# Optimization experiments

Measured on AMD Instinct MI355X. Metric: run time of the kernel, lower is better.

## Reference

```python
import jax, jax.numpy as jnp
import numpy as np

N, D, R, E = 50000, 256, 4, 800000
LN_EPS = 1e-5
NEG_INF = -1e30  # finite stand-in for -inf so softmax stays grad-safe


def _layernorm(x, g, b):
    m = x.mean(axis=-1, keepdims=True)
    v = x.var(axis=-1, keepdims=True)
    return (x - m) / jnp.sqrt(v + LN_EPS) * g + b


def setup_inputs() -> dict:
    key = jax.random.key(0)
    ks = jax.random.split(key, 8)
    s = 1.0 / np.sqrt(D).astype(np.float32)
    return {
        'rows': jax.random.randint(ks[0], (R, E), 0, N),
        'cols': jax.random.randint(ks[1], (R, E), 0, N),
        'vals': jax.random.uniform(ks[2], (R, E), jnp.float32),
        'node_emb': jax.random.normal(ks[3], (N, D), jnp.float32) * s,
        'pre_W': jax.random.normal(ks[4], (D, D), jnp.float32) * s,
        'pre_b': jnp.zeros((D,), jnp.float32),
        'ln1_g': jnp.ones((D,), jnp.float32),
        'ln1_b': jnp.zeros((D,), jnp.float32),
        'rel_W': jax.random.normal(ks[5], (R, D, D), jnp.float32) * s,
        'attn_vec': jax.random.normal(ks[6], (D,), jnp.float32) * s,
        'self_W': jax.random.normal(ks[7], (D, D), jnp.float32) * s,
        'self_b': jnp.zeros((D,), jnp.float32),
        'bias': jnp.zeros((D,), jnp.float32),
        'ln2_g': jnp.ones((D,), jnp.float32),
        'ln2_b': jnp.zeros((D,), jnp.float32),
    }


def reference(rows, cols, vals, node_emb, pre_W, pre_b, ln1_g, ln1_b, rel_W,
              attn_vec, self_W, self_b, bias, ln2_g, ln2_b):
    # active_indices = arange(N), so x_all is the full embedding table
    x_all = node_emb
    # pre_encoder: Linear -> LayerNorm -> GELU (exact erf, torch default)
    x = jax.nn.gelu(_layernorm(x_all @ pre_W + pre_b, ln1_g, ln1_b), approximate=False)
    # per-relation: relation linear then SpMM (adj_t @ x_rel) via gather + segment_sum
    msgs = []
    for i in range(R):
        x_rel = x @ rel_W[i]                              # [N, D]
        contrib = vals[i][:, None] * x_rel[cols[i]]       # [E, D]
        msgs.append(jax.ops.segment_sum(contrib, rows[i], num_segments=N))
    stacked = jnp.stack(msgs, axis=1)                     # [N, R, D]
    # semantic attention over relations
    scores = jnp.einsum('nrd,d->nr', stacked, attn_vec)   # [N, R]
    mask = jnp.any(stacked != 0, axis=2)                  # [N, R]
    attn = jax.nn.softmax(jnp.where(mask, scores, NEG_INF), axis=1)
    attn = attn * mask                                    # == nan_to_num(softmax(-inf rows))
    out = jnp.einsum('nrd,nr->nd', stacked, attn) + bias + (x @ self_W + self_b)
    out = jax.nn.gelu(out, approximate=False)
    # active_indices = arange(N): scatter into global index space is identity
    final = _layernorm(out, ln2_g, ln2_b)
    return final, attn, x_all
```

## Files before the change

kernel.cpp:

```cpp
#include <hip/hip_runtime.h>
#include <math.h>


typedef __attribute__((ext_vector_type(8))) short bf16x8;
typedef __attribute__((ext_vector_type(4))) float f32x4;
typedef unsigned long long u64;

__device__ __forceinline__ float gelu_exact(float v) {
    return 0.5f * v * (1.0f + erff(v * 0.70710678118654752f));
}
__device__ __forceinline__ unsigned short f2bf(float f) {
    unsigned u = __float_as_uint(f);
    return (unsigned short)((u + 0x7fffu + ((u >> 16) & 1u)) >> 16);
}
__device__ __forceinline__ unsigned pack2(float a, float b) {
    return (unsigned)f2bf(a) | ((unsigned)f2bf(b) << 16);
}
__device__ __forceinline__ void gload16(const void* g, void* l) {
    __builtin_amdgcn_global_load_lds(
        (const __attribute__((address_space(1))) void*)g,
        (__attribute__((address_space(3))) void*)l, 16, 0, 0);
}

__global__ __launch_bounds__(256)
void conv_emb(const float* __restrict__ ne, unsigned short* __restrict__ emb,
              float* __restrict__ outX, int total4)
{
    const int stride = gridDim.x * blockDim.x;
    for (int i = blockIdx.x * blockDim.x + threadIdx.x; i < total4; i += stride) {
        const float4 v = reinterpret_cast<const float4*>(ne)[i];
        reinterpret_cast<float4*>(outX)[i] = v;
        ushort4 h;
        h.x = f2bf(v.x); h.y = f2bf(v.y); h.z = f2bf(v.z); h.w = f2bf(v.w);
        reinterpret_cast<ushort4*>(emb)[i] = h;
    }
}

__global__ __launch_bounds__(256)
void build_bt(const float* __restrict__ relW, const float* __restrict__ selfW,
              const float* __restrict__ preW, unsigned short* __restrict__ BTm,
              unsigned short* __restrict__ BTp)
{
    const int idx = blockIdx.x * 256 + threadIdx.x;
    if (idx < 1280 * 256) {
        const int k = idx >> 8, n = idx & 255;
        const float v = (k < 1024)
            ? relW[(size_t)(k >> 8) * 65536 + (size_t)(k & 255) * 256 + n]
            : selfW[(size_t)(k - 1024) * 256 + n];
        BTm[(size_t)n * 1280 + k] = f2bf(v);
    } else {
        const int i2 = idx - 1280 * 256;
        if (i2 < 256 * 256) {
            const int k = i2 >> 8, n = i2 & 255;
            BTp[(size_t)n * 256 + k] = f2bf(preW[(size_t)k * 256 + n]);
        }
    }
}

template<int MODE>
__global__ __launch_bounds__(512)
void gemm_mfma(const unsigned short* __restrict__ a0,
               const unsigned short* __restrict__ a1,
               const unsigned short* __restrict__ a2,
               const unsigned short* __restrict__ a3,
               const unsigned short* __restrict__ a4,
               const unsigned short* __restrict__ BT,
               const float* __restrict__ bias0, const float* __restrict__ bias1,
               const float* __restrict__ lng, const float* __restrict__ lnb,
               float* __restrict__ Cout, unsigned short* __restrict__ XOut,
               int M)
{
    constexpr int K    = MODE ? 1280 : 256;
    constexpr int NSEG = MODE ? 5 : 1;

    __shared__ __align__(16) unsigned char smA[128 * 128];
    __shared__ __align__(16) unsigned char smB[256 * 128];
    __shared__ float redS[4][128];
    __shared__ float redQ[4][128];

    const int tid = threadIdx.x;
    const int w   = tid >> 6;
    const int l   = tid & 63;
    const int wm  = w >> 2, wn = w & 3;
    const int brow = blockIdx.x * 128;

    const int srow = l >> 3;
    const int sgA  = (l & 7) ^ srow;

    f32x4 acc[4][4];
#pragma unroll
    for (int mb = 0; mb < 4; ++mb)
#pragma unroll
        for (int nb = 0; nb < 4; ++nb)
            acc[mb][nb] = f32x4{0.f, 0.f, 0.f, 0.f};

    for (int seg = 0; seg < NSEG; ++seg) {
        const unsigned short* Abase =
            (MODE == 0) ? a0
                        : (seg == 0 ? a0 : seg == 1 ? a1 : seg == 2 ? a2
                                         : seg == 3 ? a3 : a4);
#pragma unroll
        for (int kk = 0; kk < 4; ++kk) {
            __syncthreads();
#pragma unroll
            for (int c = 0; c < 2; ++c) {
                const int r0 = (w * 2 + c) * 8;
                int gm = brow + r0 + srow;
                gm = min(gm, M - 1);
                gload16(Abase + ((size_t)gm << 8) + kk * 64 + sgA * 8,
                        smA + (w * 2 + c) * 1024);
            }
#pragma unroll
            for (int c = 0; c < 4; ++c) {
                const int bn = (w * 4 + c) * 8 + srow;
                gload16(BT + (size_t)bn * K + (seg * 4 + kk) * 64 + sgA * 8,
                        smB + (w * 4 + c) * 1024);
            }
            __syncthreads();

#pragma unroll
            for (int ks = 0; ks < 2; ++ks) {
                bf16x8 af[4], bf[4];
#pragma unroll
                for (int mb = 0; mb < 4; ++mb) {
                    const int row = wm * 64 + mb * 16 + (l & 15);
                    const int g   = (ks * 4 + (l >> 4)) ^ (row & 7);
                    af[mb] = *reinterpret_cast<const bf16x8*>(smA + row * 128 + g * 16);
                }
#pragma unroll
                for (int nb = 0; nb < 4; ++nb) {
                    const int row = wn * 64 + nb * 16 + (l & 15);
                    const int g   = (ks * 4 + (l >> 4)) ^ (row & 7);
                    bf[nb] = *reinterpret_cast<const bf16x8*>(smB + row * 128 + g * 16);
                }
#pragma unroll
                for (int mb = 0; mb < 4; ++mb)
#pragma unroll
                    for (int nb = 0; nb < 4; ++nb)
                        acc[mb][nb] = __builtin_amdgcn_mfma_f32_16x16x32_bf16(
                            af[mb], bf[nb], acc[mb][nb], 0, 0, 0);
            }
        }
    }

    float bb[4], gw[4], bw[4];
#pragma unroll
    for (int nb = 0; nb < 4; ++nb) {
        const int n = wn * 64 + nb * 16 + (l & 15);
        bb[nb] = bias0[n] + (MODE == 1 ? bias1[n] : 0.0f);
        gw[nb] = lng[n];
        bw[nb] = lnb[n];
    }
#pragma unroll
    for (int mb = 0; mb < 4; ++mb)
#pragma unroll
        for (int nb = 0; nb < 4; ++nb)
#pragma unroll
            for (int rg = 0; rg < 4; ++rg) {
                float v = acc[mb][nb][rg] + bb[nb];
                if (MODE == 1) v = gelu_exact(v);
                acc[mb][nb][rg] = v;
            }
#pragma unroll
    for (int mb = 0; mb < 4; ++mb)
#pragma unroll
        for (int rg = 0; rg < 4; ++rg) {
            float s = 0.f, q = 0.f;
#pragma unroll
            for (int nb = 0; nb < 4; ++nb) {
                const float v = acc[mb][nb][rg];
                s += v; q += v * v;
            }
#pragma unroll
            for (int off = 1; off < 16; off <<= 1) {
                s += __shfl_xor(s, off, 64);
                q += __shfl_xor(q, off, 64);
            }
            if ((l & 15) == 0) {
                const int row = wm * 64 + mb * 16 + (l >> 4) * 4 + rg;
                redS[wn][row] = s;
                redQ[wn][row] = q;
            }
        }
    __syncthreads();
    if (tid < 128) {
        const float s = redS[0][tid] + redS[1][tid] + redS[2][tid] + redS[3][tid];
        const float q = redQ[0][tid] + redQ[1][tid] + redQ[2][tid] + redQ[3][tid];
        const float mean = s * (1.0f / 256.0f);
        const float var  = q * (1.0f / 256.0f) - mean * mean;
        redS[0][tid] = mean;
        redQ[0][tid] = rsqrtf(var + 1e-5f);
    }
    __syncthreads();
#pragma unroll
    for (int mb = 0; mb < 4; ++mb)
#pragma unroll
        for (int rg = 0; rg < 4; ++rg) {
            const int row = wm * 64 + mb * 16 + (l >> 4) * 4 + rg;
            if (brow + row >= M) continue;
            const float mu = redS[0][row];
            const float rs = redQ[0][row];
#pragma unroll
            for (int nb = 0; nb < 4; ++nb) {
                const int n = wn * 64 + nb * 16 + (l & 15);
                const float v = (acc[mb][nb][rg] - mu) * rs * gw[nb] + bw[nb];
                if (MODE == 0)
                    XOut[((size_t)(brow + row) << 8) + n] = f2bf(gelu_exact(v));
                else
                    Cout[((size_t)(brow + row) << 8) + n] = v;
            }
        }
}

__global__ __launch_bounds__(256)
void wtilde_kernel(const float* __restrict__ relW, const float* __restrict__ av,
                   float* __restrict__ wt)
{
    __shared__ float avs[256];
    const int r = blockIdx.x, tid = threadIdx.x;
    avs[tid] = av[tid];
    __syncthreads();
    const float* W = relW + (size_t)r * 65536 + (size_t)tid * 256;
    float s = 0.f;
    for (int j = 0; j < 256; j += 4) {
        const float4 w4 = *reinterpret_cast<const float4*>(W + j);
        s += w4.x * avs[j] + w4.y * avs[j + 1] + w4.z * avs[j + 2] + w4.w * avs[j + 3];
    }
    wt[r * 256 + tid] = s;
}

__global__ __launch_bounds__(256)
void y_kernel(const unsigned short* __restrict__ XB, const float* __restrict__ wt,
              float* __restrict__ y, int Nn)
{
    const int n = blockIdx.x * 4 + (threadIdx.x >> 6);
    if (n >= Nn) return;
    const int l = threadIdx.x & 63;
    const uint2 d = *reinterpret_cast<const uint2*>(XB + ((size_t)n << 8) + l * 4);
    float xv[4];
    xv[0] = __uint_as_float(d.x << 16);
    xv[1] = __uint_as_float(d.x & 0xffff0000u);
    xv[2] = __uint_as_float(d.y << 16);
    xv[3] = __uint_as_float(d.y & 0xffff0000u);
    float s[4];
#pragma unroll
    for (int r = 0; r < 4; ++r) {
        const float4 w4 = *reinterpret_cast<const float4*>(wt + r * 256 + l * 4);
        s[r] = xv[0] * w4.x + xv[1] * w4.y + xv[2] * w4.z + xv[3] * w4.w;
#pragma unroll
        for (int off = 32; off; off >>= 1) s[r] += __shfl_xor(s[r], off, 64);
    }
    if (l == 0)
        *reinterpret_cast<float4*>(y + (size_t)n * 4) = make_float4(s[0], s[1], s[2], s[3]);
}

__global__ __launch_bounds__(256)
void hist_widbin(const int* __restrict__ rows, int* __restrict__ counts,
                 int* __restrict__ cnt_t, int RE, int E, int Nn,
                 int chunk, int NBIN)
{
    __shared__ int lh[800];
    const int blk = blockIdx.x;
    for (int i = threadIdx.x; i < NBIN; i += 256) lh[i] = 0;
    __syncthreads();
    const int e0 = blk * chunk;
    const int e1 = min(e0 + chunk, RE);
    for (int e = e0 + threadIdx.x; e < e1; e += 256) {
        const int r   = e / E;
        const int wid = r * Nn + rows[e];
        atomicAdd(&counts[wid], 1);
        atomicAdd(&lh[wid >> 8], 1);
    }
    __syncthreads();
    for (int i = threadIdx.x; i < NBIN; i += 256)
        cnt_t[i * gridDim.x + blk] = lh[i];
}

__global__ __launch_bounds__(256)
void scan_blocks(const int* __restrict__ counts, int* __restrict__ offs,
                 int* __restrict__ bsums, int n)
{
    __shared__ int sh[256];
    const int t = threadIdx.x;
    const int base = blockIdx.x * 1024 + t * 4;
    int v[4], s = 0;
#pragma unroll
    for (int j = 0; j < 4; ++j) {
        v[j] = (base + j < n) ? counts[base + j] : 0;
        s += v[j];
    }
    sh[t] = s;
    __syncthreads();
    for (int off = 1; off < 256; off <<= 1) {
        const int x = (t >= off) ? sh[t - off] : 0;
        __syncthreads();
        sh[t] += x;
        __syncthreads();
    }
    int run = sh[t] - s;
    if (t == 255) bsums[blockIdx.x] = sh[255];
#pragma unroll
    for (int j = 0; j < 4; ++j) {
        if (base + j < n) offs[base + j] = run;
        run += v[j];
    }
}

__global__ __launch_bounds__(256)
void scan_bsums(int* __restrict__ bsums, int nblk)
{
    __shared__ int sh[256];
    const int t = threadIdx.x;
    const int v = (t < nblk) ? bsums[t] : 0;
    sh[t] = v;
    __syncthreads();
    for (int off = 1; off < 256; off <<= 1) {
        const int x = (t >= off) ? sh[t - off] : 0;
        __syncthreads();
        sh[t] += x;
        __syncthreads();
    }
    if (t < nblk) bsums[t] = sh[t] - v;
}

__global__ __launch_bounds__(256)
void scan_add(int* __restrict__ offs, const int* __restrict__ bsums, int n)
{
    const int i = blockIdx.x * 256 + threadIdx.x;
    if (i >= n) return;
    offs[i] += bsums[i >> 10];
}

__global__ __launch_bounds__(256)
void scatter_coarse(const int* __restrict__ rows, const int* __restrict__ cols,
                    const float* __restrict__ vals, const int* __restrict__ ctoffs,
                    u64* __restrict__ edc, int RE, int E, int Nn,
                    int chunk, int NBIN)
{
    __shared__ int lcur[800];
    const int blk = blockIdx.x;
    for (int i = threadIdx.x; i < NBIN; i += 256)
        lcur[i] = ctoffs[i * gridDim.x + blk];
    __syncthreads();
    const int e0 = blk * chunk;
    const int e1 = min(e0 + chunk, RE);
    for (int e = e0 + threadIdx.x; e < e1; e += 256) {
        const int r   = e / E;
        const int row = rows[e];
        const int wid = r * Nn + row;
        const int pos = atomicAdd(&lcur[wid >> 8], 1);
        const unsigned vb = __float_as_uint(vals[e]);
        edc[pos] = ((u64)((vb & 0xFFFFFFFCu) | (unsigned)r) << 32)
                 | ((unsigned)row << 16) | (unsigned)cols[e];
    }
}

__global__ __launch_bounds__(256)
void scatter_fine(const u64* __restrict__ edc, const int* __restrict__ ctoffs,
                  const int* __restrict__ offs, u64* __restrict__ edata,
                  int RE, int Nn, int NB1, int NBIN)
{
    __shared__ int cur[256];
    const int bin     = blockIdx.x;
    const int widbase = bin << 8;
    const int RN      = Nn << 2;
    const int wid     = widbase + threadIdx.x;
    cur[threadIdx.x] = (wid < RN) ? offs[wid] : 0;
    __syncthreads();
    const int cs = ctoffs[bin * NB1];
    const int ce = (bin + 1 < NBIN) ? ctoffs[(bin + 1) * NB1] : RE;
    for (int j = cs + threadIdx.x; j < ce; j += 256) {
        const u64 p  = edc[j];
        const unsigned hi = (unsigned)(p >> 32);
        const unsigned lo = (unsigned)p;
        const int r   = (int)(hi & 3u);
        const int row = (int)(lo >> 16);
        const int w   = r * Nn + row;
        const int pos = atomicAdd(&cur[w - widbase], 1);
        edata[pos] = ((u64)(hi & 0xFFFFFFFCu) << 32) | (lo & 0xFFFFu);
    }
}

__global__ __launch_bounds__(256)
void score_csr(const int* __restrict__ offs, const u64* __restrict__ edata,
               const float* __restrict__ y, float* __restrict__ scores,
               int Nn, int RE)
{
    const int wid = blockIdx.x * 256 + threadIdx.x;
    const int RN  = Nn << 2;
    if (wid >= RN) return;
    const int r = wid / Nn;
    const int n = wid - r * Nn;
    const int start = offs[wid];
    const int end   = (wid + 1 < RN) ? offs[wid + 1] : RE;

    float s = 0.f;
    int j = start;
    for (; j + 3 < end; j += 4) {
        u64 e[4];
        float yv[4], vv[4];
#pragma unroll
        for (int q = 0; q < 4; ++q) e[q] = edata[j + q];
#pragma unroll
        for (int q = 0; q < 4; ++q) {
            vv[q] = __uint_as_float((unsigned)(e[q] >> 32));
            yv[q] = y[((size_t)(unsigned)(e[q] & 0xffffffffu)) * 4 + r];
        }
#pragma unroll
        for (int q = 0; q < 4; ++q) s = fmaf(vv[q], yv[q], s);
    }
    for (; j < end; ++j) {
        const u64 e0 = edata[j];
        s = fmaf(__uint_as_float((unsigned)(e0 >> 32)),
                 y[((size_t)(unsigned)(e0 & 0xffffffffu)) * 4 + r], s);
    }
    scores[(size_t)n * 4 + r] = (end > start) ? s : -1e30f;
}

__global__ __launch_bounds__(256)
void softmax4(const float* __restrict__ scores, float* __restrict__ attn, int Nn)
{
    const int n = blockIdx.x * 256 + threadIdx.x;
    if (n >= Nn) return;
    const float4 s4 = *reinterpret_cast<const float4*>(scores + (size_t)n * 4);
    float s[4] = { s4.x, s4.y, s4.z, s4.w };
    float mx = -3.0e38f;
#pragma unroll
    for (int r = 0; r < 4; ++r) mx = fmaxf(mx, s[r]);
    float ex[4], es = 0.f;
#pragma unroll
    for (int r = 0; r < 4; ++r) { ex[r] = expf(s[r] - mx); es += ex[r]; }
    const float inv = 1.0f / es;
    float4 o;
    o.x = (s[0] > -1e29f) ? ex[0] * inv : 0.0f;
    o.y = (s[1] > -1e29f) ? ex[1] * inv : 0.0f;
    o.z = (s[2] > -1e29f) ? ex[2] * inv : 0.0f;
    o.w = (s[3] > -1e29f) ? ex[3] * inv : 0.0f;
    *reinterpret_cast<float4*>(attn + (size_t)n * 4) = o;
}

__global__ __launch_bounds__(256)
void agg_csr(const int* __restrict__ offs, const u64* __restrict__ edata,
             const unsigned short* __restrict__ x, const float* __restrict__ attn,
             unsigned short* __restrict__ agg, int Nn, int RE)
{
    const int wid  = (blockIdx.x << 2) + (threadIdx.x >> 6);
    const int lane = threadIdx.x & 63;
    const int RN   = Nn << 2;
    if (wid >= RN) return;
    const int r = wid / Nn;
    const int n = wid - r * Nn;

    const int start = offs[wid];
    const int end   = (wid + 1 < RN) ? offs[wid + 1] : RE;

    float ax = 0.f, ay = 0.f, az = 0.f, aw = 0.f;
    int j = start;
    for (; j + 3 < end; j += 4) {
        u64 e[4];
        uint2 d[4];
        float v[4];
#pragma unroll
        for (int q = 0; q < 4; ++q) e[q] = edata[j + q];
#pragma unroll
        for (int q = 0; q < 4; ++q) {
            const int c = (int)(e[q] & 0xffffffffu);
            v[q] = __uint_as_float((unsigned)(e[q] >> 32));
            d[q] = *reinterpret_cast<const uint2*>(x + ((size_t)c << 8) + lane * 4);
        }
#pragma unroll
        for (int q = 0; q < 4; ++q) {
            ax = fmaf(v[q], __uint_as_float(d[q].x << 16),         ax);
            ay = fmaf(v[q], __uint_as_float(d[q].x & 0xffff0000u), ay);
            az = fmaf(v[q], __uint_as_float(d[q].y << 16),         az);
            aw = fmaf(v[q], __uint_as_float(d[q].y & 0xffff0000u), aw);
        }
    }
    for (; j < end; ++j) {
        const u64 e0 = edata[j];
        const int   c0 = (int)(e0 & 0xffffffffu);
        const float v0 = __uint_as_float((unsigned)(e0 >> 32));
        const uint2 d0 = *reinterpret_cast<const uint2*>(x + ((size_t)c0 << 8) + lane * 4);
        ax = fmaf(v0, __uint_as_float(d0.x << 16),         ax);
        ay = fmaf(v0, __uint_as_float(d0.x & 0xffff0000u), ay);
        az = fmaf(v0, __uint_as_float(d0.y << 16),         az);
        aw = fmaf(v0, __uint_as_float(d0.y & 0xffff0000u), aw);
    }

    const float sc = attn[(size_t)n * 4 + r];
    uint2 st;
    st.x = pack2(sc * ax, sc * ay);
    st.y = pack2(sc * az, sc * aw);
    *reinterpret_cast<uint2*>(agg + ((size_t)wid << 8) + lane * 4) = st;
}

extern "C" void kernel_launch(void* const* d_in, const int* in_sizes, int n_in,
                              void* d_out, int out_size, void* d_ws, size_t ws_size,
                              hipStream_t stream)
{
    const int*   rows     = (const int*)d_in[0];
    const int*   cols     = (const int*)d_in[1];
    const float* vals     = (const float*)d_in[2];
    const float* node_emb = (const float*)d_in[3];
    const float* pre_W    = (const float*)d_in[4];
    const float* pre_b    = (const float*)d_in[5];
    const float* ln1_g    = (const float*)d_in[6];
    const float* ln1_b    = (const float*)d_in[7];
    const float* rel_W    = (const float*)d_in[8];
    const float* attn_vec = (const float*)d_in[9];
    const float* self_W   = (const float*)d_in[10];
    const float* self_b   = (const float*)d_in[11];
    const float* bias     = (const float*)d_in[12];
    const float* ln2_g    = (const float*)d_in[13];
    const float* ln2_b    = (const float*)d_in[14];

    const int Dd = 256;
    const int R  = in_sizes[8] / (Dd * Dd);
    const int N  = in_sizes[3] / Dd;
    const int E  = in_sizes[0] / R;
    const int RE = R * E;
    const int RN = R * N;

    const int NB1   = 256;
    const int chunk = (RE + NB1 - 1) / NB1;
    const int NBIN  = (RN + 255) / 256;
    const int NCT   = NBIN * NB1;

    float* out  = (float*)d_out;
    float* outF = out;
    float* outA = out + (size_t)N * Dd;
    float* outX = outA + (size_t)N * R;

    char* wp = (char*)d_ws;
    auto alloc = [&](size_t bytes) {
        char* p = wp;
        wp += (bytes + 255) & ~(size_t)255;
        return p;
    };
    unsigned short* AGGS = (unsigned short*)alloc((size_t)RN * Dd * 2);
    unsigned short* XB   = (unsigned short*)alloc((size_t)N * Dd * 2);
    unsigned short* EMB  = (unsigned short*)alloc((size_t)N * Dd * 2);
    unsigned short* BTm  = (unsigned short*)alloc((size_t)Dd * 1280 * 2);
    unsigned short* BTp  = (unsigned short*)alloc((size_t)Dd * Dd * 2);
    float* WT   = (float*)alloc((size_t)R * Dd * 4);
    float* Y    = (float*)alloc((size_t)N * R * 4);
    float* SC   = (float*)alloc((size_t)N * R * 4);
    int* counts = (int*)alloc((size_t)RN * 4);
    int* offs   = (int*)alloc((size_t)RN * 4);
    int* cnt_t  = (int*)alloc((size_t)NCT * 4);
    int* ctoffs = cnt_t;
    int* bsums  = (int*)alloc(1024);
    int* bsums2 = (int*)alloc(1024);
    u64* edata  = (u64*)alloc((size_t)RE * 8);
    u64* edc    = (u64*)alloc((size_t)RE * 8);

    const int gblocks = (N + 127) / 128;
    const int nblkW   = (RN + 1023) / 1024;
    const int nblkC   = (NCT + 1023) / 1024;

    build_bt<<<(1280 * 256 + 256 * 256 + 255) / 256, 256, 0, stream>>>(
        rel_W, self_W, pre_W, BTm, BTp);
    conv_emb<<<2048, 256, 0, stream>>>(node_emb, EMB, outX, N * Dd / 4);

    gemm_mfma<0><<<gblocks, 512, 0, stream>>>(EMB, nullptr, nullptr, nullptr, nullptr,
                                              BTp, pre_b, nullptr, ln1_g, ln1_b,
                                              nullptr, XB, N);
    wtilde_kernel<<<R, 256, 0, stream>>>(rel_W, attn_vec, WT);
    y_kernel<<<(N + 3) / 4, 256, 0, stream>>>(XB, WT, Y, N);

    hipMemsetAsync(counts, 0, (size_t)RN * sizeof(int), stream);
    hist_widbin<<<NB1, 256, 0, stream>>>(rows, counts, cnt_t, RE, E, N, chunk, NBIN);
    scan_blocks<<<nblkW, 256, 0, stream>>>(counts, offs, bsums, RN);
    scan_bsums<<<1, 256, 0, stream>>>(bsums, nblkW);
    scan_add<<<(RN + 255) / 256, 256, 0, stream>>>(offs, bsums, RN);
    scan_blocks<<<nblkC, 256, 0, stream>>>(cnt_t, ctoffs, bsums2, NCT);
    scan_bsums<<<1, 256, 0, stream>>>(bsums2, nblkC);
    scan_add<<<(NCT + 255) / 256, 256, 0, stream>>>(ctoffs, bsums2, NCT);
    scatter_coarse<<<NB1, 256, 0, stream>>>(rows, cols, vals, ctoffs, edc,
                                            RE, E, N, chunk, NBIN);
    scatter_fine<<<NBIN, 256, 0, stream>>>(edc, ctoffs, offs, edata, RE, N, NB1, NBIN);

    score_csr<<<(RN + 255) / 256, 256, 0, stream>>>(offs, edata, Y, SC, N, RE);
    softmax4<<<(N + 255) / 256, 256, 0, stream>>>(SC, outA, N);

    agg_csr<<<(RN + 3) / 4, 256, 0, stream>>>(offs, edata, XB, outA, AGGS, N, RE);

    gemm_mfma<1><<<gblocks, 512, 0, stream>>>(AGGS, AGGS + (size_t)N * Dd,
                                              AGGS + (size_t)2 * N * Dd,
                                              AGGS + (size_t)3 * N * Dd, XB,
                                              BTm, bias, self_b, ln2_g, ln2_b,
                                              outF, nullptr, N);
}
```

Baseline: 671.8 us.

## Compute per-row CSR offsets inside scatter_fine and aggregate with packed fp16 FMAs

Removes the global per-row histogram atomics, the memset and the three-kernel scan over per-(relation,row) counts. scatter_fine now computes those offsets itself with a shared-memory count and scan inside each bin. The GEMM epilogue also writes an fp16 copy of x, which agg_csr uses to gather 16-byte chunks per lane, with two half-waves each taking alternate edges and accumulating with packed half2 FMAs before a cross-half shuffle reduction. Edge loads and the aggregate stores are marked nontemporal. This cuts launches and global atomics and halves the aggregation instruction count, but fp16 accumulation loses precision and the extra fp16 buffer adds write traffic.

New measurement: 589.3 us. 12.3% less time.

```diff
diff --git a/kernel.cpp b/kernel.cpp
--- a/kernel.cpp
+++ b/kernel.cpp
@@ -1,9 +1,11 @@
 #include <hip/hip_runtime.h>
+#include <hip/hip_fp16.h>
 #include <math.h>
 
 
 typedef __attribute__((ext_vector_type(8))) short bf16x8;
 typedef __attribute__((ext_vector_type(4))) float f32x4;
+typedef __attribute__((ext_vector_type(4))) unsigned u32x4;
 typedef unsigned long long u64;
 
 __device__ __forceinline__ float gelu_exact(float v) {
@@ -15,6 +17,12 @@
 }
 __device__ __forceinline__ unsigned pack2(float a, float b) {
     return (unsigned)f2bf(a) | ((unsigned)f2bf(b) << 16);
+}
+__device__ __forceinline__ unsigned short f2h(float f) {
+    return __half_as_ushort(__float2half(f));
+}
+__device__ __forceinline__ __half2 u2h2(unsigned u) {
+    union { unsigned u; __half2 h; } c; c.u = u; return c.h;
 }
 __device__ __forceinline__ void gload16(const void* g, void* l) {
     __builtin_amdgcn_global_load_lds(
@@ -68,7 +76,7 @@
                const float* __restrict__ bias0, const float* __restrict__ bias1,
                const float* __restrict__ lng, const float* __restrict__ lnb,
                float* __restrict__ Cout, unsigned short* __restrict__ XOut,
-               int M)
+               unsigned short* __restrict__ XH, int M)
 {
     constexpr int K    = MODE ? 1280 : 256;
     constexpr int NSEG = MODE ? 5 : 1;
@@ -204,10 +212,13 @@
             for (int nb = 0; nb < 4; ++nb) {
                 const int n = wn * 64 + nb * 16 + (l & 15);
                 const float v = (acc[mb][nb][rg] - mu) * rs * gw[nb] + bw[nb];
-                if (MODE == 0)
-                    XOut[((size_t)(brow + row) << 8) + n] = f2bf(gelu_exact(v));
-                else
+                if (MODE == 0) {
+                    const float gv = gelu_exact(v);
+                    XOut[((size_t)(brow + row) << 8) + n] = f2bf(gv);
+                    XH[((size_t)(brow + row) << 8) + n]   = f2h(gv);
+                } else {
                     Cout[((size_t)(brow + row) << 8) + n] = v;
+                }
             }
         }
 }
@@ -255,9 +266,8 @@
 }
 
 __global__ __launch_bounds__(256)
-void hist_widbin(const int* __restrict__ rows, int* __restrict__ counts,
-                 int* __restrict__ cnt_t, int RE, int E, int Nn,
-                 int chunk, int NBIN)
+void hist_bin(const int* __restrict__ rows, int* __restrict__ cnt_t,
+              int RE, int E, int Nn, int chunk, int NBIN)
 {
     __shared__ int lh[800];
     const int blk = blockIdx.x;
@@ -268,7 +278,6 @@
     for (int e = e0 + threadIdx.x; e < e1; e += 256) {
         const int r   = e / E;
         const int wid = r * Nn + rows[e];
-        atomicAdd(&counts[wid], 1);
         atomicAdd(&lh[wid >> 8], 1);
     }
     __syncthreads();
@@ -357,25 +366,47 @@
 
 __global__ __launch_bounds__(256)
 void scatter_fine(const u64* __restrict__ edc, const int* __restrict__ ctoffs,
-                  const int* __restrict__ offs, u64* __restrict__ edata,
+                  int* __restrict__ offs, u64* __restrict__ edata,
                   int RE, int Nn, int NB1, int NBIN)
 {
+    __shared__ int cnt[256];
     __shared__ int cur[256];
     const int bin     = blockIdx.x;
     const int widbase = bin << 8;
     const int RN      = Nn << 2;
-    const int wid     = widbase + threadIdx.x;
-    cur[threadIdx.x] = (wid < RN) ? offs[wid] : 0;
+    const int t       = threadIdx.x;
+    cnt[t] = 0;
     __syncthreads();
     const int cs = ctoffs[bin * NB1];
     const int ce = (bin + 1 < NBIN) ? ctoffs[(bin + 1) * NB1] : RE;
-    for (int j = cs + threadIdx.x; j < ce; j += 256) {
+    for (int j = cs + t; j < ce; j += 256) {
+        const u64 p = edc[j];
+        const unsigned hi = (unsigned)(p >> 32);
+        const unsigned lo = (unsigned)p;
+        const int w = (int)(hi & 3u) * Nn + (int)(lo >> 16);
+        atomicAdd(&cnt[w - widbase], 1);
+    }
+    __syncthreads();
+    const int v = cnt[t];
+    cur[t] = v;
+    __syncthreads();
+    for (int off = 1; off < 256; off <<= 1) {
+        const int x = (t >= off) ? cur[t - off] : 0;
+        __syncthreads();
+        cur[t] += x;
+        __syncthreads();
+    }
+    const int excl = cur[t] - v;
+    const int wid  = widbase + t;
+    if (wid < RN) offs[wid] = cs + excl;
+    __syncthreads();
+    cur[t] = cs + excl;
+    __syncthreads();
+    for (int j = cs + t; j < ce; j += 256) {
         const u64 p  = edc[j];
         const unsigned hi = (unsigned)(p >> 32);
         const unsigned lo = (unsigned)p;
-        const int r   = (int)(hi & 3u);
-        const int row = (int)(lo >> 16);
-        const int w   = r * Nn + row;
+        const int w   = (int)(hi & 3u) * Nn + (int)(lo >> 16);
         const int pos = atomicAdd(&cur[w - widbase], 1);
         edata[pos] = ((u64)(hi & 0xFFFFFFFCu) << 32) | (lo & 0xFFFFu);
     }
@@ -400,7 +431,7 @@
         u64 e[4];
         float yv[4], vv[4];
 #pragma unroll
-        for (int q = 0; q < 4; ++q) e[q] = edata[j + q];
+        for (int q = 0; q < 4; ++q) e[q] = __builtin_nontemporal_load(edata + j + q);
 #pragma unroll
         for (int q = 0; q < 4; ++q) {
             vv[q] = __uint_as_float((unsigned)(e[q] >> 32));
@@ -441,11 +472,13 @@
 
 __global__ __launch_bounds__(256)
 void agg_csr(const int* __restrict__ offs, const u64* __restrict__ edata,
-             const unsigned short* __restrict__ x, const float* __restrict__ attn,
+             const unsigned short* __restrict__ xh, const float* __restrict__ attn,
              unsigned short* __restrict__ agg, int Nn, int RE)
 {
     const int wid  = (blockIdx.x << 2) + (threadIdx.x >> 6);
     const int lane = threadIdx.x & 63;
+    const int half = lane >> 5;
+    const int sub  = lane & 31;
     const int RN   = Nn << 2;
     if (wid >= RN) return;
     const int r = wid / Nn;
@@ -454,44 +487,56 @@
     const int start = offs[wid];
     const int end   = (wid + 1 < RN) ? offs[wid + 1] : RE;
 
-    float ax = 0.f, ay = 0.f, az = 0.f, aw = 0.f;
-    int j = start;
-    for (; j + 3 < end; j += 4) {
-        u64 e[4];
-        uint2 d[4];
-        float v[4];
-#pragma unroll
-        for (int q = 0; q < 4; ++q) e[q] = edata[j + q];
-#pragma unroll
-        for (int q = 0; q < 4; ++q) {
-            const int c = (int)(e[q] & 0xffffffffu);
-            v[q] = __uint_as_float((unsigned)(e[q] >> 32));
-            d[q] = *reinterpret_cast<const uint2*>(x + ((size_t)c << 8) + lane * 4);
-        }
-#pragma unroll
-        for (int q = 0; q < 4; ++q) {
-            ax = fmaf(v[q], __uint_as_float(d[q].x << 16),         ax);
-            ay = fmaf(v[q], __uint_as_float(d[q].x & 0xffff0000u), ay);
-            az = fmaf(v[q], __uint_as_float(d[q].y << 16),         az);
-            aw = fmaf(v[q], __uint_as_float(d[q].y & 0xffff0000u), aw);
-        }
-    }
-    for (; j < end; ++j) {
-        const u64 e0 = edata[j];
-        const int   c0 = (int)(e0 & 0xffffffffu);
-        const float v0 = __uint_as_float((unsigned)(e0 >> 32));
-        const uint2 d0 = *reinterpret_cast<const uint2*>(x + ((size_t)c0 << 8) + lane * 4);
-        ax = fmaf(v0, __uint_as_float(d0.x << 16),         ax);
-        ay = fmaf(v0, __uint_as_float(d0.x & 0xffff0000u), ay);
-        az = fmaf(v0, __uint_as_float(d0.y << 16),         az);
-        aw = fmaf(v0, __uint_as_float(d0.y & 0xffff0000u), aw);
-    }
-
-    const float sc = attn[(size_t)n * 4 + r];
-    uint2 st;
-    st.x = pack2(sc * ax, sc * ay);
-    st.y = pack2(sc * az, sc * aw);
-    *reinterpret_cast<uint2*>(agg + ((size_t)wid << 8) + lane * 4) = st;
+    __half2 acc0 = __float2half2_rn(0.f), acc1 = acc0, acc2 = acc0, acc3 = acc0;
+
+    int j = start + half;
+    for (; j + 2 < end; j += 4) {
+        const u64 e0 = __builtin_nontemporal_load(edata + j);
+        const u64 e1 = __builtin_nontemporal_load(edata + j + 2);
+        const int c0 = (int)(e0 & 0xffffffffu);
+        const int c1 = (int)(e1 & 0xffffffffu);
+        const __half2 v0 = __float2half2_rn(__uint_as_float((unsigned)(e0 >> 32)));
+        const __half2 v1 = __float2half2_rn(__uint_as_float((unsigned)(e1 >> 32)));
+        const uint4 d0 = *reinterpret_cast<const uint4*>(xh + ((size_t)c0 << 8) + sub * 8);
+        const uint4 d1 = *reinterpret_cast<const uint4*>(xh + ((size_t)c1 << 8) + sub * 8);
+        acc0 = __hfma2(v0, u2h2(d0.x), acc0);
+        acc1 = __hfma2(v0, u2h2(d0.y), acc1);
+        acc2 = __hfma2(v0, u2h2(d0.z), acc2);
+        acc3 = __hfma2(v0, u2h2(d0.w), acc3);
+        acc0 = __hfma2(v1, u2h2(d1.x), acc0);
+        acc1 = __hfma2(v1, u2h2(d1.y), acc1);
+        acc2 = __hfma2(v1, u2h2(d1.z), acc2);
+        acc3 = __hfma2(v1, u2h2(d1.w), acc3);
+    }
+    for (; j < end; j += 2) {
+        const u64 e0 = __builtin_nontemporal_load(edata + j);
+        const int c0 = (int)(e0 & 0xffffffffu);
+        const __half2 v0 = __float2half2_rn(__uint_as_float((unsigned)(e0 >> 32)));
+        const uint4 d0 = *reinterpret_cast<const uint4*>(xh + ((size_t)c0 << 8) + sub * 8);
+        acc0 = __hfma2(v0, u2h2(d0.x), acc0);
+        acc1 = __hfma2(v0, u2h2(d0.y), acc1);
+        acc2 = __hfma2(v0, u2h2(d0.z), acc2);
+        acc3 = __hfma2(v0, u2h2(d0.w), acc3);
+    }
+
+    float a[8];
+    a[0] = __low2float(acc0); a[1] = __high2float(acc0);
+    a[2] = __low2float(acc1); a[3] = __high2float(acc1);
+    a[4] = __low2float(acc2); a[5] = __high2float(acc2);
+    a[6] = __low2float(acc3); a[7] = __high2float(acc3);
+#pragma unroll
+    for (int i = 0; i < 8; ++i) a[i] += __shfl_xor(a[i], 32, 64);
+
+    if (half == 0) {
+        const float sc = attn[(size_t)n * 4 + r];
+        u32x4 st;
+        st.x = pack2(sc * a[0], sc * a[1]);
+        st.y = pack2(sc * a[2], sc * a[3]);
+        st.z = pack2(sc * a[4], sc * a[5]);
+        st.w = pack2(sc * a[6], sc * a[7]);
+        __builtin_nontemporal_store(
+            st, reinterpret_cast<u32x4*>(agg + ((size_t)wid << 8) + sub * 8));
+    }
 }
 
 extern "C" void kernel_launch(void* const* d_in, const int* in_sizes, int n_in,
@@ -539,23 +584,21 @@
     };
     unsigned short* AGGS = (unsigned short*)alloc((size_t)RN * Dd * 2);
     unsigned short* XB   = (unsigned short*)alloc((size_t)N * Dd * 2);
+    unsigned short* XH   = (unsigned short*)alloc((size_t)N * Dd * 2);
     unsigned short* EMB  = (unsigned short*)alloc((size_t)N * Dd * 2);
     unsigned short* BTm  = (unsigned short*)alloc((size_t)Dd * 1280 * 2);
     unsigned short* BTp  = (unsigned short*)alloc((size_t)Dd * Dd * 2);
     float* WT   = (float*)alloc((size_t)R * Dd * 4);
     float* Y    = (float*)alloc((size_t)N * R * 4);
     float* SC   = (float*)alloc((size_t)N * R * 4);
-    int* counts = (int*)alloc((size_t)RN * 4);
     int* offs   = (int*)alloc((size_t)RN * 4);
     int* cnt_t  = (int*)alloc((size_t)NCT * 4);
     int* ctoffs = cnt_t;
-    int* bsums  = (int*)alloc(1024);
     int* bsums2 = (int*)alloc(1024);
     u64* edata  = (u64*)alloc((size_t)RE * 8);
     u64* edc    = (u64*)alloc((size_t)RE * 8);
 
     const int gblocks = (N + 127) / 128;
-    const int nblkW   = (RN + 1023) / 1024;
     const int nblkC   = (NCT + 1023) / 1024;
 
     build_bt<<<(1280 * 256 + 256 * 256 + 255) / 256, 256, 0, stream>>>(
@@ -564,15 +607,11 @@
 
     gemm_mfma<0><<<gblocks, 512, 0, stream>>>(EMB, nullptr, nullptr, nullptr, nullptr,
                                               BTp, pre_b, nullptr, ln1_g, ln1_b,
-                                              nullptr, XB, N);
+                                              nullptr, XB, XH, N);
     wtilde_kernel<<<R, 256, 0, stream>>>(rel_W, attn_vec, WT);
     y_kernel<<<(N + 3) / 4, 256, 0, stream>>>(XB, WT, Y, N);
 
-    hipMemsetAsync(counts, 0, (size_t)RN * sizeof(int), stream);
-    hist_widbin<<<NB1, 256, 0, stream>>>(rows, counts, cnt_t, RE, E, N, chunk, NBIN);
-    scan_blocks<<<nblkW, 256, 0, stream>>>(counts, offs, bsums, RN);
-    scan_bsums<<<1, 256, 0, stream>>>(bsums, nblkW);
-    scan_add<<<(RN + 255) / 256, 256, 0, stream>>>(offs, bsums, RN);
+    hist_bin<<<NB1, 256, 0, stream>>>(rows, cnt_t, RE, E, N, chunk, NBIN);
     scan_blocks<<<nblkC, 256, 0, stream>>>(cnt_t, ctoffs, bsums2, NCT);
     scan_bsums<<<1, 256, 0, stream>>>(bsums2, nblkC);
     scan_add<<<(NCT + 255) / 256, 256, 0, stream>>>(ctoffs, bsums2, NCT);
@@ -583,11 +622,11 @@
     score_csr<<<(RN + 255) / 256, 256, 0, stream>>>(offs, edata, Y, SC, N, RE);
     softmax4<<<(N + 255) / 256, 256, 0, stream>>>(SC, outA, N);
 
-    agg_csr<<<(RN + 3) / 4, 256, 0, stream>>>(offs, edata, XB, outA, AGGS, N, RE);
+    agg_csr<<<(RN + 3) / 4, 256, 0, stream>>>(offs, edata, XH, outA, AGGS, N, RE);
 
     gemm_mfma<1><<<gblocks, 512, 0, stream>>>(AGGS, AGGS + (size_t)N * Dd,
                                               AGGS + (size_t)2 * N * Dd,
                                               AGGS + (size_t)3 * N * Dd, XB,
                                               BTm, bias, self_b, ln2_g, ln2_b,
-                                              outF, nullptr, N);
-}
+                                              outF, nullptr, nullptr, N);
+}
```
